# Kernel optimization log

Hardware: AMD Instinct MI355X
Metric: run time of the kernel (lower is better)

Reference implementation:

```python
import jax, jax.numpy as jnp
import numpy as np

B, N, NPOINT, NSAMPLE = 8, 8192, 512, 32
D, NHEAD, NLAYERS, DIM_OUT = 128, 8, 4, 256
HD = D // NHEAD
DFF = 2 * D
EPS = 1e-5

_gather = jax.vmap(lambda p, i: p[i])  # p: [N,C], i: [...] -> [...,C]


def _ln(x, g, b):
    m = jnp.mean(x, -1, keepdims=True)
    v = jnp.var(x, -1, keepdims=True)
    return (x - m) / jnp.sqrt(v + EPS) * g + b


def _fps(pts):
    # pts: [B,N,3] -> centroid indices [B,NPOINT]; start index 0 (torch uses randint)
    Bb, Nn, _ = pts.shape
    def step(carry, _):
        dist, far = carry
        cen = jax.vmap(lambda p, f: p[f])(pts, far)[:, None, :]  # [B,1,3]
        dist = jnp.minimum(dist, jnp.sum((pts - cen) ** 2, -1))
        return (dist, jnp.argmax(dist, -1)), far
    init = (jnp.full((Bb, Nn), 1e10, pts.dtype), jnp.zeros((Bb,), jnp.int32))
    _, cents = jax.lax.scan(step, init, None, length=NPOINT)
    return cents.T  # [B,NPOINT]


def _interp_linear(x, n_out):
    # x: [B,C,S] -> [B,C,n_out], linear, align_corners=True
    S = x.shape[-1]
    pos = jnp.arange(n_out) * ((S - 1) / (n_out - 1))
    i0 = jnp.floor(pos).astype(jnp.int32)
    i1 = jnp.minimum(i0 + 1, S - 1)
    w = (pos - i0).astype(x.dtype)
    return x[..., i0] * (1 - w) + x[..., i1] * w


def _layer(x, p):
    wqkv, bqkv, wo, bo, g1, be1, w1, bf1, w2, bf2, g2, be2 = p
    Bt, K, _ = x.shape
    qkv = x @ wqkv.T + bqkv
    q, k, v = jnp.split(qkv, 3, axis=-1)
    q = q.reshape(Bt, K, NHEAD, HD)
    k = k.reshape(Bt, K, NHEAD, HD)
    v = v.reshape(Bt, K, NHEAD, HD)
    att = jax.nn.softmax(jnp.einsum('bqhd,bkhd->bhqk', q, k) / jnp.sqrt(jnp.float32(HD)), axis=-1)
    o = jnp.einsum('bhqk,bkhd->bqhd', att, v).reshape(Bt, K, D)
    x = _ln(x + o @ wo.T + bo, g1, be1)
    ff = jax.nn.relu(x @ w1.T + bf1) @ w2.T + bf2
    return _ln(x + ff, g2, be2)


def setup_inputs():
    key = jax.random.key(0)
    ks = jax.random.split(key, 10)
    w = lambda k, s: jax.random.normal(k, s, jnp.float32) * 0.02
    return {
        'xyz': jax.random.normal(ks[0], (B, 3, N), jnp.float32),
        'features': jax.random.normal(ks[1], (B, D, N), jnp.float32),
        'pe_w1': w(ks[2], (D // 2, 3)), 'pe_b1': jnp.zeros((D // 2,), jnp.float32),
        'bn_gamma': jnp.ones((D // 2,), jnp.float32), 'bn_beta': jnp.zeros((D // 2,), jnp.float32),
        'bn_mean': jnp.zeros((D // 2,), jnp.float32), 'bn_var': jnp.ones((D // 2,), jnp.float32),
        'pe_w2': w(ks[3], (D, D // 2)), 'pe_b2': jnp.zeros((D,), jnp.float32),
        'attn_wqkv': w(ks[4], (NLAYERS, 3 * D, D)), 'attn_bqkv': jnp.zeros((NLAYERS, 3 * D), jnp.float32),
        'attn_wo': w(ks[5], (NLAYERS, D, D)), 'attn_bo': jnp.zeros((NLAYERS, D), jnp.float32),
        'ln1_g': jnp.ones((NLAYERS, D), jnp.float32), 'ln1_b': jnp.zeros((NLAYERS, D), jnp.float32),
        'ffn_w1': w(ks[6], (NLAYERS, DFF, D)), 'ffn_b1': jnp.zeros((NLAYERS, DFF), jnp.float32),
        'ffn_w2': w(ks[7], (NLAYERS, D, DFF)), 'ffn_b2': jnp.zeros((NLAYERS, D), jnp.float32),
        'ln2_g': jnp.ones((NLAYERS, D), jnp.float32), 'ln2_b': jnp.zeros((NLAYERS, D), jnp.float32),
        'fc_w': w(ks[8], (DIM_OUT, D)), 'fc_b': jnp.zeros((DIM_OUT,), jnp.float32),
    }


def reference(xyz, features, pe_w1, pe_b1, bn_gamma, bn_beta, bn_mean, bn_var, pe_w2, pe_b2,
              attn_wqkv, attn_bqkv, attn_wo, attn_bo, ln1_g, ln1_b,
              ffn_w1, ffn_b1, ffn_w2, ffn_b2, ln2_g, ln2_b, fc_w, fc_b):
    pts = jnp.transpose(xyz, (0, 2, 1))                 # [B,N,3]
    fps_idx = _fps(pts)                                 # [B,S]
    new_xyz = _gather(pts, fps_idx)                     # [B,S,3]
    # kNN: squared distances [B,S,N]
    d2 = (jnp.sum(new_xyz ** 2, -1)[..., None] + jnp.sum(pts ** 2, -1)[:, None, :]
          - 2.0 * jnp.einsum('bsc,bnc->bsn', new_xyz, pts))
    _, gidx = jax.lax.top_k(-d2, NSAMPLE)               # [B,S,K]
    gxyz = _gather(pts, gidx)                           # [B,S,K,3]
    gfeat = _gather(jnp.transpose(features, (0, 2, 1)), gidx)  # [B,S,K,D]
    # positional encoding: 1x1 conv -> BN (eval) -> relu -> 1x1 conv
    h = gxyz @ pe_w1.T + pe_b1
    h = (h - bn_mean) / jnp.sqrt(bn_var + EPS) * bn_gamma + bn_beta
    pe = jax.nn.relu(h) @ pe_w2.T + pe_b2               # [B,S,K,D]
    x = (gfeat + pe).reshape(B * NPOINT, NSAMPLE, D)    # tokens: K neighbors per center
    layer_params = (attn_wqkv, attn_bqkv, attn_wo, attn_bo, ln1_g, ln1_b,
                    ffn_w1, ffn_b1, ffn_w2, ffn_b2, ln2_g, ln2_b)
    x, _ = jax.lax.scan(lambda c, p: (_layer(c, p), None), x, layer_params)
    x = x.reshape(B, NPOINT, NSAMPLE, D).max(axis=2)    # max-pool over neighbors [B,S,D]
    out = jnp.transpose(x @ fc_w.T + fc_b, (0, 2, 1))   # [B,DIM_OUT,S]
    out_up = _interp_linear(out, N)                     # [B,DIM_OUT,N]
    return jnp.transpose(new_xyz, (0, 2, 1)), out_up
```

## Files before the change

kernel.cpp:

```cpp
#include <hip/hip_runtime.h>
#include <math.h>

constexpr int CB  = 8;
constexpr int CN  = 8192;
constexpr int CS  = 512;
constexpr int CK  = 32;
constexpr int CD  = 128;
constexpr int CF  = 256;
constexpr int CO  = 256;
constexpr float CEPS = 1e-5f;

typedef __attribute__((ext_vector_type(8)))  short short8;
typedef __attribute__((ext_vector_type(4)))  float f32x4;
typedef __attribute__((ext_vector_type(16))) float f32x16;
#define MFMA16(a,b,c) __builtin_amdgcn_mfma_f32_16x16x32_bf16(a,b,c,0,0,0)
#define MFMA32(a,b,c) __builtin_amdgcn_mfma_f32_32x32x16_bf16(a,b,c,0,0,0)

__device__ __forceinline__ ushort f2b(float f){
  unsigned u = __builtin_bit_cast(unsigned, f);
  u = u + 0x7fffu + ((u >> 16) & 1u);
  return (ushort)(u >> 16);
}

__global__ __launch_bounds__(512)
void fps_kernel(const float* __restrict__ xyz, int* __restrict__ fps_idx)
{
#pragma clang fp contract(off)
  __shared__ __align__(16) float4 p4[CN];
  __shared__ unsigned long long wred[2][8];
  const int b = blockIdx.x, t = threadIdx.x;
  const int w = t >> 6, lane = t & 63;
  const float* xb = xyz + (size_t)b*3*CN;
  float px[16], py[16], pz[16], dist[16];
  #pragma unroll
  for (int j=0;j<16;j++){
    const int i = t + 512*j;
    px[j] = xb[i]; py[j] = xb[CN+i]; pz[j] = xb[2*CN+i];
    dist[j] = 1e10f;
    p4[i] = make_float4(px[j], py[j], pz[j], 0.f);
  }
  __syncthreads();
  int far = 0, par = 0;
  float4 c = p4[0];
  for (int it = 0; it < CS; ++it){
    if (t == 0) fps_idx[b*CS + it] = far;
    unsigned long long kk[16];
    #pragma unroll
    for (int j=0;j<16;j++){
      const float dx = px[j]-c.x, dy = py[j]-c.y, dz = pz[j]-c.z;
      const float d2 = (dx*dx + dy*dy) + dz*dz;
      const float nd = fminf(dist[j], d2);
      dist[j] = nd;
      kk[j] = ((unsigned long long)__builtin_bit_cast(unsigned, nd) << 32)
              | (unsigned)(8191 - (t + 512*j));
    }
    #pragma unroll
    for (int st=1; st<16; st<<=1)
      #pragma unroll
      for (int j=0;j<16;j+=2*st)
        kk[j] = kk[j] >= kk[j+st] ? kk[j] : kk[j+st];
    unsigned long long key = kk[0];
    #pragma unroll
    for (int off=1; off<=32; off<<=1){
      const unsigned long long o = __shfl_xor(key, off);
      key = o > key ? o : key;
    }
    if (lane == 0) wred[par][w] = key;
    __syncthreads();
    unsigned long long k2 = wred[par][lane & 7];
    #pragma unroll
    for (int off=1; off<=4; off<<=1){
      const unsigned long long o = __shfl_xor(k2, off);
      k2 = o > k2 ? o : k2;
    }
    far = 8191 - (int)(k2 & 0xFFFFFFFFu);
    c = p4[far];
    par ^= 1;
  }
}

__global__ __launch_bounds__(256)
void knn_kernel(const float* __restrict__ xyz, const int* __restrict__ fps_idx,
                int* __restrict__ gidx)
{
#pragma clang fp contract(off)
  __shared__ float wv[4];
  __shared__ int   wi[4];
  __shared__ int   win_sh;
  const int blk = blockIdx.x, t = threadIdx.x;
  const int b = blk >> 9;
  const int s = blk & 511;
  const float* xb = xyz + (size_t)b*3*CN;
  const int cidx = fps_idx[b*CS + s];
  const float cx = xb[cidx], cy = xb[CN+cidx], cz = xb[2*CN+cidx];
  const float cn2 = (cx*cx + cy*cy) + cz*cz;
  float dv[32];
  float mv = 1e30f; int mi = 0;
  #pragma unroll
  for (int j=0;j<32;j++){
    const int i = t + 256*j;
    const float x = xb[i], y = xb[CN+i], z = xb[2*CN+i];
    const float pn2 = (x*x + y*y) + z*z;
    const float dot = (cx*x + cy*y) + cz*z;
    const float d2 = (cn2 + pn2) - 2.0f*dot;
    dv[j] = d2;
    if (d2 < mv || (d2 == mv && i < mi)){ mv = d2; mi = i; }
  }
  for (int k=0;k<CK;k++){
    float v = mv; int i = mi;
    #pragma unroll
    for (int off=32; off>=1; off>>=1){
      const float ov = __shfl_xor(v, off);
      const int   oi = __shfl_xor(i, off);
      if (ov < v || (ov == v && oi < i)){ v = ov; i = oi; }
    }
    if ((t & 63) == 0){ wv[t>>6] = v; wi[t>>6] = i; }
    __syncthreads();
    if (t == 0){
      #pragma unroll
      for (int w=1;w<4;w++)
        if (wv[w] < v || (wv[w] == v && wi[w] < i)){ v = wv[w]; i = wi[w]; }
      win_sh = i;
      gidx[(size_t)blk*CK + k] = i;
    }
    __syncthreads();
    const int win = win_sh;
    if ((win & 255) == t){
      const int jw = win >> 8;
      #pragma unroll
      for (int j=0;j<32;j++) if (j == jw) dv[j] = 1e30f;
      mv = 1e30f; mi = 0;
      #pragma unroll
      for (int j=0;j<32;j++){
        const int i2 = t + 256*j;
        if (dv[j] < mv || (dv[j] == mv && i2 < mi)){ mv = dv[j]; mi = i2; }
      }
    }
  }
}

__global__ __launch_bounds__(256)
void newxyz_kernel(const float* __restrict__ xyz, const int* __restrict__ fps_idx,
                   float* __restrict__ out0)
{
  const int idx = blockIdx.x*256 + threadIdx.x;
  if (idx >= CB*3*CS) return;
  const int s = idx & 511;
  const int c = (idx >> 9) % 3;
  const int b = idx / (3*CS);
  const int n = fps_idx[b*CS + s];
  out0[idx] = xyz[(size_t)b*3*CN + (size_t)c*CN + n];
}

__global__ __launch_bounds__(256)
void transpose_kernel(const float* __restrict__ f, float* __restrict__ ft)
{
  __shared__ float tile[32][33];
  const int b = blockIdx.z, d0 = blockIdx.y*32, n0 = blockIdx.x*32;
  const int tx = threadIdx.x, ty = threadIdx.y;
  const float* fb = f + (size_t)b*CD*CN;
  #pragma unroll
  for (int r=0;r<32;r+=8) tile[ty+r][tx] = fb[(size_t)(d0+ty+r)*CN + n0+tx];
  __syncthreads();
  float* ftb = ft + (size_t)b*CN*CD;
  #pragma unroll
  for (int r=0;r<32;r+=8) ftb[(size_t)(n0+ty+r)*CD + d0+tx] = tile[tx][ty+r];
}

__global__ __launch_bounds__(256)
void pe_kernel(const float* __restrict__ xyz, const float* __restrict__ features,
               const float* __restrict__ featT, const int* __restrict__ gidx,
               const float* __restrict__ pe_w1, const float* __restrict__ pe_b1,
               const float* __restrict__ bn_g, const float* __restrict__ bn_b,
               const float* __restrict__ bn_m, const float* __restrict__ bn_v,
               const float* __restrict__ pe_w2, const float* __restrict__ pe_b2,
               float* __restrict__ xout)
{
  __shared__ __align__(16) float w2s[CD*68];
  __shared__ __align__(16) float hr[CK*68];
  __shared__ int idxs[CK];
  __shared__ float gx[CK], gy[CK], gz[CK];
  const int g = blockIdx.x, t = threadIdx.x;
  const int b = g >> 9;
  for (int i=t; i<CD*64; i+=256) w2s[(i>>6)*68 + (i&63)] = pe_w2[i];
  if (t < CK){
    const int id = gidx[(size_t)g*CK + t];
    idxs[t] = id;
    const float* xb = xyz + (size_t)b*3*CN;
    gx[t] = xb[id]; gy[t] = xb[CN+id]; gz[t] = xb[2*CN+id];
  }
  __syncthreads();
  for (int v=t; v<CK*64; v+=256){
    const int k = v>>6, j = v&63;
    float h = ((gx[k]*pe_w1[j*3] + gy[k]*pe_w1[j*3+1]) + gz[k]*pe_w1[j*3+2]) + pe_b1[j];
    h = (h - bn_m[j]) / sqrtf(bn_v[j] + CEPS) * bn_g[j] + bn_b[j];
    hr[k*68+j] = fmaxf(h, 0.f);
  }
  __syncthreads();
  const float* fb  = features + (size_t)b*CD*CN;
  const float* ftb = featT ? (featT + (size_t)b*CN*CD) : nullptr;
  for (int p=t; p<CK*CD; p+=256){
    const int k = p>>7, d = p&127;
    const float4* hp = (const float4*)(hr  + k*68);
    const float4* wp = (const float4*)(w2s + d*68);
    float acc = 0.f;
    #pragma unroll
    for (int j=0;j<16;j++){
      const float4 a = hp[j], w = wp[j];
      acc += a.x*w.x; acc += a.y*w.y; acc += a.z*w.z; acc += a.w*w.w;
    }
    acc += pe_b2[d];
    const float gf = ftb ? ftb[(size_t)idxs[k]*CD + d] : fb[(size_t)d*CN + idxs[k]];
    xout[(size_t)g*CK*CD + p] = gf + acc;
  }
}

__global__ __launch_bounds__(256)
void wprep_kernel(const float* __restrict__ wqkv, const float* __restrict__ wo,
                  const float* __restrict__ w1,   const float* __restrict__ w2,
                  ushort* __restrict__ dst)
{
  const int tid = blockIdx.x*256 + threadIdx.x;
  const int l = tid & 63;
  const int f = tid >> 6;
  const int L = f >> 8;
  const int r = f & 255;
  const float* src; int stride, nt, kt;
  if (r < 96)      { nt = r>>2;        kt = r&3;        src = wqkv + (size_t)L*384*128; stride = 128; }
  else if (r < 128){ nt = (r-96)>>2;   kt = (r-96)&3;   src = wo   + (size_t)L*128*128; stride = 128; }
  else if (r < 192){ nt = (r-128)>>2;  kt = (r-128)&3;  src = w1   + (size_t)L*256*128; stride = 128; }
  else             { nt = (r-192)>>3;  kt = (r-192)&7;  src = w2   + (size_t)L*128*256; stride = 256; }
  const int n = nt*16 + (l & 15);
  const int k = kt*32 + (l >> 4)*8;
  const float* p = src + (size_t)n*stride + k;
  uint4 o;
  o.x = (unsigned)f2b(p[0]) | ((unsigned)f2b(p[1])<<16);
  o.y = (unsigned)f2b(p[2]) | ((unsigned)f2b(p[3])<<16);
  o.z = (unsigned)f2b(p[4]) | ((unsigned)f2b(p[5])<<16);
  o.w = (unsigned)f2b(p[6]) | ((unsigned)f2b(p[7])<<16);
  *(uint4*)(dst + (size_t)tid*8) = o;
}

__device__ __forceinline__ void ln_inplace(float* x32s, ushort* xbv,
                                           const float* __restrict__ gamma,
                                           const float* __restrict__ beta, int t)
{
  const int r = t >> 3, j = t & 7;
  float v[16]; float s = 0.f;
  #pragma unroll
  for (int i=0;i<16;i++){ v[i] = x32s[r*132 + j + 8*i]; s += v[i]; }
  #pragma unroll
  for (int off=1; off<8; off<<=1) s += __shfl_xor(s, off);
  const float mean = s * (1.f/128.f);
  float var = 0.f;
  #pragma unroll
  for (int i=0;i<16;i++){ const float d = v[i]-mean; var += d*d; }
  #pragma unroll
  for (int off=1; off<8; off<<=1) var += __shfl_xor(var, off);
  const float inv = 1.f / sqrtf(var*(1.f/128.f) + CEPS);
  #pragma unroll
  for (int i=0;i<16;i++){
    const int d = j + 8*i;
    const float o = (v[i]-mean)*inv*gamma[d] + beta[d];
    x32s[r*132 + d] = o;
    xbv[r*136 + d] = f2b(o);
  }
}

__global__ __launch_bounds__(256, 2)
void layer_mfma_kernel(float* __restrict__ xbuf, const ushort* __restrict__ wf,
                       const float* __restrict__ bqkv, const float* __restrict__ bo,
                       const float* __restrict__ g1, const float* __restrict__ b1v,
                       const float* __restrict__ bf1, const float* __restrict__ bf2,
                       const float* __restrict__ g2, const float* __restrict__ b2v)
{
  __shared__ __align__(16) float  x32s[32*132];
  __shared__ __align__(16) ushort xbv [32*136];
  __shared__ __align__(16) ushort qk  [32*264];
  __shared__ __align__(16) ushort vT  [128*40];
  __shared__ __align__(16) ushort Pb  [4*32*40];
  const int g = blockIdx.x, t = threadIdx.x;
  const int w = t>>6, l = t&63;
  const int l15 = l&15, q4 = l>>4, l31 = l&31, hi = l>>5;
  float* xg = xbuf + (size_t)g*1024*4;
  const uint4* wfv = (const uint4*)wf;

  for (int i=t;i<1024;i+=256){
    const float4 v = ((const float4*)xg)[i];
    const int r = i>>5, c = (i&31)*4;
    *(float4*)&x32s[r*132 + c] = v;
    uint2 p;
    p.x = (unsigned)f2b(v.x) | ((unsigned)f2b(v.y)<<16);
    p.y = (unsigned)f2b(v.z) | ((unsigned)f2b(v.w)<<16);
    *(uint2*)&xbv[r*136 + c] = p;
  }
  __syncthreads();

  {
    short8 a[2][4];
    #pragma unroll
    for (int mt=0;mt<2;mt++)
      #pragma unroll
      for (int kt=0;kt<4;kt++)
        a[mt][kt] = __builtin_bit_cast(short8, *(const uint4*)&xbv[(l15+16*mt)*136 + kt*32 + q4*8]);
    for (int i=0;i<6;i++){
      const int nt = w + 4*i;
      const int n  = nt*16 + l15;
      f32x4 a0 = {0.f,0.f,0.f,0.f}, a1 = {0.f,0.f,0.f,0.f};
      #pragma unroll
      for (int kt=0;kt<4;kt++){
        const short8 b = __builtin_bit_cast(short8, wfv[(nt*4+kt)*64 + l]);
        a0 = MFMA16(a[0][kt], b, a0);
        a1 = MFMA16(a[1][kt], b, a1);
      }
      const float bias = bqkv[n];
      if (nt < 16){
        #pragma unroll
        for (int i2=0;i2<4;i2++){
          qk[(q4*4+i2   )*264 + n] = f2b(a0[i2]+bias);
          qk[(q4*4+i2+16)*264 + n] = f2b(a1[i2]+bias);
        }
      } else {
        const int d = n - 256;
        uint2 p0, p1;
        p0.x = (unsigned)f2b(a0[0]+bias) | ((unsigned)f2b(a0[1]+bias)<<16);
        p0.y = (unsigned)f2b(a0[2]+bias) | ((unsigned)f2b(a0[3]+bias)<<16);
        p1.x = (unsigned)f2b(a1[0]+bias) | ((unsigned)f2b(a1[1]+bias)<<16);
        p1.y = (unsigned)f2b(a1[2]+bias) | ((unsigned)f2b(a1[3]+bias)<<16);
        *(uint2*)&vT[d*40 + q4*4]      = p0;
        *(uint2*)&vT[d*40 + 16 + q4*4] = p1;
      }
    }
  }
  __syncthreads();

  for (int hh=0; hh<2; hh++){
    const int h = 2*w + hh;
    const short8 ka = __builtin_bit_cast(short8, *(const uint4*)&qk[l31*264 + 128 + h*16 + hi*8]);
    const short8 qb = __builtin_bit_cast(short8, *(const uint4*)&qk[l31*264 +       h*16 + hi*8]);
    f32x16 s;
    #pragma unroll
    for (int i=0;i<16;i++) s[i] = 0.f;
    s = MFMA32(ka, qb, s);
    float e[16]; float mx = -1e30f;
    #pragma unroll
    for (int i=0;i<16;i++){ e[i] = s[i]*0.25f; mx = fmaxf(mx, e[i]); }
    mx = fmaxf(mx, __shfl_xor(mx, 32));
    float sum = 0.f;
    #pragma unroll
    for (int i=0;i<16;i++){ e[i] = __expf(e[i]-mx); sum += e[i]; }
    sum += __shfl_xor(sum, 32);
    const float inv = 1.f/sum;
    #pragma unroll
    for (int j=0;j<4;j++){
      uint2 p;
      p.x = (unsigned)f2b(e[4*j  ]*inv) | ((unsigned)f2b(e[4*j+1]*inv)<<16);
      p.y = (unsigned)f2b(e[4*j+2]*inv) | ((unsigned)f2b(e[4*j+3]*inv)<<16);
      *(uint2*)&Pb[w*1280 + l31*40 + j*8 + hi*4] = p;
    }
    const short8 bv = __builtin_bit_cast(short8, *(const uint4*)&vT[(h*16+l15)*40 + q4*8]);
    #pragma unroll
    for (int mt=0;mt<2;mt++){
      const short8 ap = __builtin_bit_cast(short8, *(const uint4*)&Pb[w*1280 + (l15+16*mt)*40 + q4*8]);
      f32x4 o = {0.f,0.f,0.f,0.f};
      o = MFMA16(ap, bv, o);
      #pragma unroll
      for (int i2=0;i2<4;i2++)
        xbv[(16*mt + q4*4 + i2)*136 + h*16 + l15] = f2b(o[i2]);
    }
  }
  __syncthreads();

  {
    short8 a[2][4];
    #pragma unroll
    for (int mt=0;mt<2;mt++)
      #pragma unroll
      for (int kt=0;kt<4;kt++)
        a[mt][kt] = __builtin_bit_cast(short8, *(const uint4*)&xbv[(l15+16*mt)*136 + kt*32 + q4*8]);
    for (int i=0;i<2;i++){
      const int nt = w + 4*i;
      const int n  = nt*16 + l15;
      f32x4 a0 = {0.f,0.f,0.f,0.f}, a1 = {0.f,0.f,0.f,0.f};
      #pragma unroll
      for (int kt=0;kt<4;kt++){
        const short8 b = __builtin_bit_cast(short8, wfv[(96 + nt*4+kt)*64 + l]);
        a0 = MFMA16(a[0][kt], b, a0);
        a1 = MFMA16(a[1][kt], b, a1);
      }
      const float bias = bo[n];
      #pragma unroll
      for (int i2=0;i2<4;i2++){
        x32s[(q4*4+i2   )*132 + n] += a0[i2] + bias;
        x32s[(q4*4+i2+16)*132 + n] += a1[i2] + bias;
      }
    }
  }
  __syncthreads();
  ln_inplace(x32s, xbv, g1, b1v, t);
  __syncthreads();

  {
    short8 a[2][4];
    #pragma unroll
    for (int mt=0;mt<2;mt++)
      #pragma unroll
      for (int kt=0;kt<4;kt++)
        a[mt][kt] = __builtin_bit_cast(short8, *(const uint4*)&xbv[(l15+16*mt)*136 + kt*32 + q4*8]);
    for (int i=0;i<4;i++){
      const int nt = w + 4*i;
      const int n  = nt*16 + l15;
      f32x4 a0 = {0.f,0.f,0.f,0.f}, a1 = {0.f,0.f,0.f,0.f};
      #pragma unroll
      for (int kt=0;kt<4;kt++){
        const short8 b = __builtin_bit_cast(short8, wfv[(128 + nt*4+kt)*64 + l]);
        a0 = MFMA16(a[0][kt], b, a0);
        a1 = MFMA16(a[1][kt], b, a1);
      }
      const float bias = bf1[n];
      #pragma unroll
      for (int i2=0;i2<4;i2++){
        qk[(q4*4+i2   )*264 + n] = f2b(fmaxf(a0[i2]+bias, 0.f));
        qk[(q4*4+i2+16)*264 + n] = f2b(fmaxf(a1[i2]+bias, 0.f));
      }
    }
  }
  __syncthreads();

  {
    short8 a[2][8];
    #pragma unroll
    for (int mt=0;mt<2;mt++)
      #pragma unroll
      for (int kt=0;kt<8;kt++)
        a[mt][kt] = __builtin_bit_cast(short8, *(const uint4*)&qk[(l15+16*mt)*264 + kt*32 + q4*8]);
    for (int i=0;i<2;i++){
      const int nt = w + 4*i;
      const int n  = nt*16 + l15;
      f32x4 a0 = {0.f,0.f,0.f,0.f}, a1 = {0.f,0.f,0.f,0.f};
      #pragma unroll
      for (int kt=0;kt<8;kt++){
        const short8 b = __builtin_bit_cast(short8, wfv[(192 + nt*8+kt)*64 + l]);
        a0 = MFMA16(a[0][kt], b, a0);
        a1 = MFMA16(a[1][kt], b, a1);
      }
      const float bias = bf2[n];
      #pragma unroll
      for (int i2=0;i2<4;i2++){
        x32s[(q4*4+i2   )*132 + n] += a0[i2] + bias;
        x32s[(q4*4+i2+16)*132 + n] += a1[i2] + bias;
      }
    }
  }
  __syncthreads();
  ln_inplace(x32s, xbv, g2, b2v, t);
  __syncthreads();

  for (int i=t;i<1024;i+=256){
    const int r = i>>5, c = (i&31)*4;
    ((float4*)xg)[i] = *(const float4*)&x32s[r*132 + c];
  }
}

__global__ __launch_bounds__(256)
void poolfc_kernel(const float* __restrict__ xbuf, const float* __restrict__ fc_w,
                   const float* __restrict__ fc_b, float* __restrict__ fcout)
{
  __shared__ __align__(16) float pooled[CD];
  const int gg = blockIdx.x, t = threadIdx.x;
  const float* xg = xbuf + (size_t)gg*CK*CD;
  if (t < CD){
    float m = -1e30f;
    for (int k=0;k<CK;k++) m = fmaxf(m, xg[(size_t)k*CD + t]);
    pooled[t] = m;
  }
  __syncthreads();
  const float* wr = fc_w + (size_t)t*CD;
  float acc = 0.f;
  const float4* pp = (const float4*)pooled;
  for (int i=0;i<CD/4;i++){
    const float4 w4 = *(const float4*)(wr + 4*i);
    const float4 p4 = pp[i];
    acc += p4.x*w4.x; acc += p4.y*w4.y; acc += p4.z*w4.z; acc += p4.w*w4.w;
  }
  acc += fc_b[t];
  const int b = gg >> 9, s = gg & 511;
  fcout[((size_t)b*CS + s)*CO + t] = acc;
}

__global__ __launch_bounds__(256)
void interp_kernel(const float* __restrict__ fcout, float* __restrict__ out1)
{
  const int idx = blockIdx.x*256 + threadIdx.x;
  const int n  = idx & (CN-1);
  const int bo = idx >> 13;
  const int b  = bo >> 8, o = bo & 255;
  const double pos = (double)n * ((double)(CS-1)/(double)(CN-1));
  const int i0 = (int)pos;
  const int i1 = min(i0+1, CS-1);
  const float w = (float)(pos - (double)i0);
  const float v0 = fcout[((size_t)b*CS + i0)*CO + o];
  const float v1 = fcout[((size_t)b*CS + i1)*CO + o];
  out1[idx] = v0*(1.f - w) + v1*w;
}

extern "C" void kernel_launch(void* const* d_in, const int* in_sizes, int n_in,
                              void* d_out, int out_size, void* d_ws, size_t ws_size,
                              hipStream_t stream)
{
  (void)in_sizes; (void)n_in; (void)out_size;
  const float* xyz      = (const float*)d_in[0];
  const float* features = (const float*)d_in[1];
  const float* pe_w1    = (const float*)d_in[2];
  const float* pe_b1    = (const float*)d_in[3];
  const float* bn_g     = (const float*)d_in[4];
  const float* bn_b     = (const float*)d_in[5];
  const float* bn_m     = (const float*)d_in[6];
  const float* bn_v     = (const float*)d_in[7];
  const float* pe_w2    = (const float*)d_in[8];
  const float* pe_b2    = (const float*)d_in[9];
  const float* wqkv     = (const float*)d_in[10];
  const float* bqkv     = (const float*)d_in[11];
  const float* wo       = (const float*)d_in[12];
  const float* bo       = (const float*)d_in[13];
  const float* g1       = (const float*)d_in[14];
  const float* b1       = (const float*)d_in[15];
  const float* w1       = (const float*)d_in[16];
  const float* bf1      = (const float*)d_in[17];
  const float* w2       = (const float*)d_in[18];
  const float* bf2      = (const float*)d_in[19];
  const float* g2       = (const float*)d_in[20];
  const float* b2       = (const float*)d_in[21];
  const float* fc_w     = (const float*)d_in[22];
  const float* fc_b     = (const float*)d_in[23];

  char* ws = (char*)d_ws;
  int*    fps_idx = (int*)(ws);
  int*    gidx    = (int*)(ws + (16u<<10));
  ushort* wfrag   = (ushort*)(ws + (1u<<20));
  float*  xbuf    = (float*)(ws + (2u<<20));
  float*  fcout   = (float*)(ws + (66u<<20));
  float*  featT   = (float*)(ws + (70u<<20));
  const bool useT = ws_size >= ((size_t)102<<20);

  float* out0 = (float*)d_out;
  float* out1 = out0 + CB*3*CS;

  fps_kernel<<<CB, 512, 0, stream>>>(xyz, fps_idx);
  knn_kernel<<<CB*CS, 256, 0, stream>>>(xyz, fps_idx, gidx);
  newxyz_kernel<<<(CB*3*CS + 255)/256, 256, 0, stream>>>(xyz, fps_idx, out0);
  wprep_kernel<<<256, 256, 0, stream>>>(wqkv, wo, w1, w2, wfrag);
  if (useT){
    dim3 tb(32, 8), tg(CN/32, CD/32, CB);
    transpose_kernel<<<tg, tb, 0, stream>>>(features, featT);
  }
  pe_kernel<<<CB*CS, 256, 0, stream>>>(xyz, features, useT ? featT : nullptr, gidx,
                                       pe_w1, pe_b1, bn_g, bn_b, bn_m, bn_v,
                                       pe_w2, pe_b2, xbuf);
  for (int L=0; L<4; L++){
    layer_mfma_kernel<<<CB*CS, 256, 0, stream>>>(xbuf,
        wfrag + (size_t)L*131072,
        bqkv + (size_t)L*3*CD, bo + (size_t)L*CD,
        g1 + (size_t)L*CD, b1 + (size_t)L*CD,
        bf1 + (size_t)L*CF, bf2 + (size_t)L*CD,
        g2 + (size_t)L*CD, b2 + (size_t)L*CD);
  }
  poolfc_kernel<<<CB*CS, 256, 0, stream>>>(xbuf, fc_w, fc_b, fcout);
  interp_kernel<<<(CB*CO*CN)/256, 256, 0, stream>>>(fcout, out1);
}
```

Before: 1.482 ms.

## Use DPP wave reductions in FPS/kNN and register-tile the positional-encoding matmul

Replaces shuffle-based 64-bit max/min reductions in the FPS and kNN kernels with DPP row/bcast reductions. kNN now uses packed sortable (distance, index) keys and a double-buffered per-wave reduction slot, which removes one __syncthreads per selection step. The PE kernel's second linear layer becomes a 4x4 register-tiled outer product with vectorized float4 feature gathers and stores. The aim is to cut per-iteration reduction latency and barrier count in the serial FPS/kNN loops and to raise data reuse in PE. The changes rely on exact DPP broadcast semantics and on the key encoding keeping tie-breaking identical.

Measured after the change: 1.443 ms. 2.6% less time.

```diff
diff --git a/kernel.cpp b/kernel.cpp
--- a/kernel.cpp
+++ b/kernel.cpp
@@ -22,6 +22,48 @@
   return (ushort)(u >> 16);
 }
 
+template<int CTRL, int RM>
+__device__ __forceinline__ unsigned long long dpp64(unsigned long long k){
+  int lo = (int)(unsigned)k;
+  int hi = (int)(unsigned)(k >> 32);
+  int plo = __builtin_amdgcn_update_dpp(lo, lo, CTRL, RM, 0xF, false);
+  int phi = __builtin_amdgcn_update_dpp(hi, hi, CTRL, RM, 0xF, false);
+  return ((unsigned long long)(unsigned)phi << 32) | (unsigned)plo;
+}
+__device__ __forceinline__ unsigned long long wave_max64(unsigned long long k){
+  unsigned long long p;
+  p = dpp64<0xB1,0xF>(k); k = p > k ? p : k;
+  p = dpp64<0x4E,0xF>(k); k = p > k ? p : k;
+  p = dpp64<0x140,0xF>(k); k = p > k ? p : k;
+  p = dpp64<0x141,0xF>(k); k = p > k ? p : k;
+  p = dpp64<0x142,0xA>(k); k = p > k ? p : k;
+  p = dpp64<0x143,0xC>(k); k = p > k ? p : k;
+  return k;
+}
+__device__ __forceinline__ unsigned long long wave_min64(unsigned long long k){
+  unsigned long long p;
+  p = dpp64<0xB1,0xF>(k); k = p < k ? p : k;
+  p = dpp64<0x4E,0xF>(k); k = p < k ? p : k;
+  p = dpp64<0x140,0xF>(k); k = p < k ? p : k;
+  p = dpp64<0x141,0xF>(k); k = p < k ? p : k;
+  p = dpp64<0x142,0xA>(k); k = p < k ? p : k;
+  p = dpp64<0x143,0xC>(k); k = p < k ? p : k;
+  return k;
+}
+__device__ __forceinline__ unsigned long long oct_max64(unsigned long long k){
+  unsigned long long p;
+  p = dpp64<0xB1,0xF>(k); k = p > k ? p : k;
+  p = dpp64<0x4E,0xF>(k); k = p > k ? p : k;
+  p = dpp64<0x141,0xF>(k); k = p > k ? p : k;
+  return k;
+}
+__device__ __forceinline__ unsigned long long quad_min64(unsigned long long k){
+  unsigned long long p;
+  p = dpp64<0xB1,0xF>(k); k = p < k ? p : k;
+  p = dpp64<0x4E,0xF>(k); k = p < k ? p : k;
+  return k;
+}
+
 __global__ __launch_bounds__(512)
 void fps_kernel(const float* __restrict__ xyz, int* __restrict__ fps_idx)
 {
@@ -59,20 +101,12 @@
       #pragma unroll
       for (int j=0;j<16;j+=2*st)
         kk[j] = kk[j] >= kk[j+st] ? kk[j] : kk[j+st];
-    unsigned long long key = kk[0];
-    #pragma unroll
-    for (int off=1; off<=32; off<<=1){
-      const unsigned long long o = __shfl_xor(key, off);
-      key = o > key ? o : key;
-    }
+    unsigned long long key = wave_max64(kk[0]);
+    key = __shfl(key, 63);
     if (lane == 0) wred[par][w] = key;
     __syncthreads();
     unsigned long long k2 = wred[par][lane & 7];
-    #pragma unroll
-    for (int off=1; off<=4; off<<=1){
-      const unsigned long long o = __shfl_xor(k2, off);
-      k2 = o > k2 ? o : k2;
-    }
+    k2 = oct_max64(k2);
     far = 8191 - (int)(k2 & 0xFFFFFFFFu);
     c = p4[far];
     par ^= 1;
@@ -84,18 +118,16 @@
                 int* __restrict__ gidx)
 {
 #pragma clang fp contract(off)
-  __shared__ float wv[4];
-  __shared__ int   wi[4];
-  __shared__ int   win_sh;
+  __shared__ unsigned long long wredk[2][4];
   const int blk = blockIdx.x, t = threadIdx.x;
+  const int w = t >> 6, l = t & 63;
   const int b = blk >> 9;
   const int s = blk & 511;
   const float* xb = xyz + (size_t)b*3*CN;
   const int cidx = fps_idx[b*CS + s];
   const float cx = xb[cidx], cy = xb[CN+cidx], cz = xb[2*CN+cidx];
   const float cn2 = (cx*cx + cy*cy) + cz*cz;
-  float dv[32];
-  float mv = 1e30f; int mi = 0;
+  unsigned long long kv[32];
   #pragma unroll
   for (int j=0;j<32;j++){
     const int i = t + 256*j;
@@ -103,39 +135,45 @@
     const float pn2 = (x*x + y*y) + z*z;
     const float dot = (cx*x + cy*y) + cz*z;
     const float d2 = (cn2 + pn2) - 2.0f*dot;
-    dv[j] = d2;
-    if (d2 < mv || (d2 == mv && i < mi)){ mv = d2; mi = i; }
-  }
+    unsigned u = __builtin_bit_cast(unsigned, d2);
+    u ^= (unsigned)((int)u >> 31) | 0x80000000u;
+    kv[j] = ((unsigned long long)u << 32) | (unsigned)i;
+  }
+  unsigned long long mv;
+  {
+    unsigned long long tmp[16];
+    #pragma unroll
+    for (int j=0;j<16;j++) tmp[j] = kv[j] < kv[j+16] ? kv[j] : kv[j+16];
+    #pragma unroll
+    for (int st=8; st>=1; st>>=1)
+      #pragma unroll
+      for (int j=0;j<st;j++) tmp[j] = tmp[j] < tmp[j+st] ? tmp[j] : tmp[j+st];
+    mv = tmp[0];
+  }
+  int par = 0;
   for (int k=0;k<CK;k++){
-    float v = mv; int i = mi;
-    #pragma unroll
-    for (int off=32; off>=1; off>>=1){
-      const float ov = __shfl_xor(v, off);
-      const int   oi = __shfl_xor(i, off);
-      if (ov < v || (ov == v && oi < i)){ v = ov; i = oi; }
-    }
-    if ((t & 63) == 0){ wv[t>>6] = v; wi[t>>6] = i; }
+    unsigned long long v = wave_min64(mv);
+    v = __shfl(v, 63);
+    if (l == 0) wredk[par][w] = v;
     __syncthreads();
-    if (t == 0){
-      #pragma unroll
-      for (int w=1;w<4;w++)
-        if (wv[w] < v || (wv[w] == v && wi[w] < i)){ v = wv[w]; i = wi[w]; }
-      win_sh = i;
-      gidx[(size_t)blk*CK + k] = i;
-    }
-    __syncthreads();
-    const int win = win_sh;
+    unsigned long long k2 = wredk[par][l & 3];
+    k2 = quad_min64(k2);
+    const int win = (int)(k2 & 0xFFFFFFFFu);
+    if (t == 0) gidx[(size_t)blk*CK + k] = win;
     if ((win & 255) == t){
       const int jw = win >> 8;
       #pragma unroll
-      for (int j=0;j<32;j++) if (j == jw) dv[j] = 1e30f;
-      mv = 1e30f; mi = 0;
-      #pragma unroll
-      for (int j=0;j<32;j++){
-        const int i2 = t + 256*j;
-        if (dv[j] < mv || (dv[j] == mv && i2 < mi)){ mv = dv[j]; mi = i2; }
-      }
-    }
+      for (int j=0;j<32;j++) if (j == jw) kv[j] = ~0ull;
+      unsigned long long tmp[16];
+      #pragma unroll
+      for (int j=0;j<16;j++) tmp[j] = kv[j] < kv[j+16] ? kv[j] : kv[j+16];
+      #pragma unroll
+      for (int st=8; st>=1; st>>=1)
+        #pragma unroll
+        for (int j=0;j<st;j++) tmp[j] = tmp[j] < tmp[j+st] ? tmp[j] : tmp[j+st];
+      mv = tmp[0];
+    }
+    par ^= 1;
   }
 }
 
@@ -197,21 +235,43 @@
     hr[k*68+j] = fmaxf(h, 0.f);
   }
   __syncthreads();
+  const int kt = t >> 5, dt = t & 31;
+  const int k0 = kt*4, d0 = dt*4;
+  float acc[4][4];
+  #pragma unroll
+  for (int a=0;a<4;a++)
+    #pragma unroll
+    for (int bb=0;bb<4;bb++) acc[a][bb] = 0.f;
+  for (int j=0;j<16;j++){
+    float4 h4[4], w4[4];
+    #pragma unroll
+    for (int a=0;a<4;a++) h4[a] = *(const float4*)&hr[(k0+a)*68 + j*4];
+    #pragma unroll
+    for (int bb=0;bb<4;bb++) w4[bb] = *(const float4*)&w2s[(d0+bb)*68 + j*4];
+    #pragma unroll
+    for (int a=0;a<4;a++)
+      #pragma unroll
+      for (int bb=0;bb<4;bb++){
+        acc[a][bb] += h4[a].x*w4[bb].x; acc[a][bb] += h4[a].y*w4[bb].y;
+        acc[a][bb] += h4[a].z*w4[bb].z; acc[a][bb] += h4[a].w*w4[bb].w;
+      }
+  }
+  const float4 b2v = *(const float4*)&pe_b2[d0];
   const float* fb  = features + (size_t)b*CD*CN;
   const float* ftb = featT ? (featT + (size_t)b*CN*CD) : nullptr;
-  for (int p=t; p<CK*CD; p+=256){
-    const int k = p>>7, d = p&127;
-    const float4* hp = (const float4*)(hr  + k*68);
-    const float4* wp = (const float4*)(w2s + d*68);
-    float acc = 0.f;
-    #pragma unroll
-    for (int j=0;j<16;j++){
-      const float4 a = hp[j], w = wp[j];
-      acc += a.x*w.x; acc += a.y*w.y; acc += a.z*w.z; acc += a.w*w.w;
-    }
-    acc += pe_b2[d];
-    const float gf = ftb ? ftb[(size_t)idxs[k]*CD + d] : fb[(size_t)d*CN + idxs[k]];
-    xout[(size_t)g*CK*CD + p] = gf + acc;
+  #pragma unroll
+  for (int a=0;a<4;a++){
+    const int id = idxs[k0+a];
+    float4 gf;
+    if (ftb) gf = *(const float4*)&ftb[(size_t)id*CD + d0];
+    else gf = make_float4(fb[(size_t)(d0+0)*CN+id], fb[(size_t)(d0+1)*CN+id],
+                          fb[(size_t)(d0+2)*CN+id], fb[(size_t)(d0+3)*CN+id]);
+    float4 o;
+    o.x = gf.x + (acc[a][0] + b2v.x);
+    o.y = gf.y + (acc[a][1] + b2v.y);
+    o.z = gf.z + (acc[a][2] + b2v.z);
+    o.w = gf.w + (acc[a][3] + b2v.w);
+    *(float4*)&xout[(size_t)g*4096 + (size_t)(k0+a)*128 + d0] = o;
   }
 }
 
```
